# Performance work log

Measured on AMD Instinct MI355X. Metric: run time of the kernel, lower is better.

Reference implementation:

```python
import jax, jax.numpy as jnp
import numpy as np

N_NODES, N_FEAT, HIDDEN, N_EDGES, N_GRAPHS = 50000, 128, 64, 800000, 64
BN_EPS = 1e-5


def setup_inputs() -> dict:
    key = jax.random.key(0)
    ks = jax.random.split(key, 12)
    x = jax.random.normal(ks[0], (N_NODES, N_FEAT), jnp.float32)
    edge_index = jax.random.randint(ks[1], (2, N_EDGES), 0, N_NODES, jnp.int32)
    batch = jnp.sort(jax.random.randint(ks[2], (N_NODES,), 0, N_GRAPHS, jnp.int32))
    s_in = 1.0 / np.sqrt(N_FEAT)
    s_h = 1.0 / np.sqrt(HIDDEN)
    return {
        "x": x,
        "edge_index": edge_index,
        "batch": batch,
        "W_in": jax.random.normal(ks[3], (HIDDEN, N_FEAT), jnp.float32) * s_in,
        "W1": jax.random.normal(ks[4], (HIDDEN, N_FEAT), jnp.float32) * s_in,
        "b1": jnp.zeros((HIDDEN,), jnp.float32),
        "Ws": jax.random.normal(ks[5], (4, HIDDEN, HIDDEN), jnp.float32) * s_h,
        "bs": jnp.zeros((4, HIDDEN), jnp.float32),
        "bn_gamma": jnp.ones((5, HIDDEN), jnp.float32),
        "bn_beta": jnp.zeros((5, HIDDEN), jnp.float32),
        "bn_mean": jnp.zeros((5, HIDDEN), jnp.float32),
        "bn_var": jnp.ones((5, HIDDEN), jnp.float32),
        "lin_w": jax.random.normal(ks[6], (1, HIDDEN), jnp.float32) * s_h,
        "lin_b": jnp.zeros((1,), jnp.float32),
    }


def reference(x, edge_index, batch, W_in, W1, b1, Ws, bs, bn_gamma, bn_beta, bn_mean, bn_var, lin_w, lin_b):
    N = x.shape[0]
    # add self loops (GCNConv default), symmetric normalization D^-1/2 (A+I) D^-1/2
    loop = jnp.arange(N, dtype=edge_index.dtype)
    src = jnp.concatenate([edge_index[0], loop])  # [E+N]
    dst = jnp.concatenate([edge_index[1], loop])
    deg = jax.ops.segment_sum(jnp.ones_like(dst, jnp.float32), dst, num_segments=N)
    dinv = jax.lax.rsqrt(deg)  # deg >= 1 due to self-loops
    norm = dinv[src] * dinv[dst]  # [E+N]

    def gcn(h, W, b):
        h = h @ W.T                          # [N, H]
        msg = h[src] * norm[:, None]          # gather + edge scaling
        out = jax.ops.segment_sum(msg, dst, num_segments=N)  # scatter-add
        return out + b

    def bn(h, i):
        # eval-mode BatchNorm1d with running stats
        return (h - bn_mean[i]) * (bn_gamma[i] * jax.lax.rsqrt(bn_var[i] + BN_EPS)) + bn_beta[i]

    identity = x @ W_in.T  # input projection for residual
    # layer 1 (dropout = identity in eval)
    h = jax.nn.relu(bn(gcn(x, W1, b1), 0)) + identity
    # layers 2-4 with residual
    for i in range(3):
        h = jax.nn.relu(bn(gcn(h, Ws[i], bs[i]), i + 1)) + h
    # layer 5, no residual afterwards
    h = jax.nn.relu(bn(gcn(h, Ws[3], bs[3]), 4))

    # global mean pool over graphs
    sums = jax.ops.segment_sum(h, batch, num_segments=N_GRAPHS)
    cnts = jax.ops.segment_sum(jnp.ones((N,), jnp.float32), batch, num_segments=N_GRAPHS)
    pooled = sums / jnp.maximum(cnts, 1.0)[:, None]  # [G, H]
    return pooled @ lin_w.T + lin_b  # [G, 1]
```

## Files before the change

kernel.cpp:

```cpp
#include <hip/hip_runtime.h>
#include <hip/hip_fp16.h>

#define N_NODES 50000
#define N_FEAT  128
#define HID     64
#define N_EDGES 800000
#define N_GRAPHS 64
#define MAXDEG  64
#define BN_EPS  1e-5f
#define NB256(n) (((n) + 255) / 256)

__global__ __launch_bounds__(256) void k_zero(int* fill) {
    int i = blockIdx.x * 256 + threadIdx.x;
    if (i < N_NODES) fill[i] = 0;
}

#define GE_NB 2500
__global__ __launch_bounds__(256) void k_gemmedge(const int* __restrict__ ei,
                                                  int* fill, unsigned short* __restrict__ colp,
                                                  const float* __restrict__ x,
                                                  const float* __restrict__ W_in,
                                                  const float* __restrict__ W1,
                                                  float* __restrict__ h,
                                                  __half* __restrict__ g16) {
    __shared__ float4 Wt[2][8 * 65];
    __shared__ float4 xs[20 * 32];
    const int bid = blockIdx.x;
    const int t = threadIdx.x;

    const int ebase = bid * 320;
    int s1 = ei[ebase + t];
    int d1 = ei[N_EDGES + ebase + t];
    int k1 = atomicAdd(&fill[d1], 1);
    int s2 = 0, d2 = 0, k2 = MAXDEG;
    if (t < 64) {
        s2 = ei[ebase + 256 + t];
        d2 = ei[N_EDGES + ebase + 256 + t];
        k2 = atomicAdd(&fill[d2], 1);
    }

    const float4* W0v = (const float4*)W_in;
    const float4* W1v = (const float4*)W1;
    const int h2a = t >> 3, k4a = t & 7;
    const int h2b = h2a + 32;
    float4 w0a = W0v[h2a * 32 + k4a];
    float4 w1a = W1v[h2a * 32 + k4a];
    float4 w0b = W0v[h2b * 32 + k4a];
    float4 w1b = W1v[h2b * 32 + k4a];

    const int base = bid * 20;
    const float4* xv = (const float4*)(x + (long long)base * N_FEAT);
    for (int i = t; i < 20 * 32; i += 256) xs[i] = xv[i];

    const int hh = t & 63;
    const int ng = t >> 6;
    float4 a0[5], a1[5];
#pragma unroll
    for (int j = 0; j < 5; ++j) {
        a0[j] = make_float4(0.f, 0.f, 0.f, 0.f);
        a1[j] = make_float4(0.f, 0.f, 0.f, 0.f);
    }

    for (int c = 0; c < 32; c += 8) {
        __syncthreads();
        Wt[0][k4a * 65 + h2a] = w0a;  Wt[1][k4a * 65 + h2a] = w1a;
        Wt[0][k4a * 65 + h2b] = w0b;  Wt[1][k4a * 65 + h2b] = w1b;
        if (c + 8 < 32) {
            w0a = W0v[h2a * 32 + c + 8 + k4a]; w1a = W1v[h2a * 32 + c + 8 + k4a];
            w0b = W0v[h2b * 32 + c + 8 + k4a]; w1b = W1v[h2b * 32 + c + 8 + k4a];
        }
        __syncthreads();
#pragma unroll
        for (int k4 = 0; k4 < 8; ++k4) {
            float4 w0 = Wt[0][k4 * 65 + hh];
            float4 w1 = Wt[1][k4 * 65 + hh];
#pragma unroll
            for (int j = 0; j < 5; ++j) {
                float4 xx = xs[(ng + 4 * j) * 32 + c + k4];
                a0[j].x += w0.x * xx.x; a0[j].y += w0.y * xx.y;
                a0[j].z += w0.z * xx.z; a0[j].w += w0.w * xx.w;
                a1[j].x += w1.x * xx.x; a1[j].y += w1.y * xx.y;
                a1[j].z += w1.z * xx.z; a1[j].w += w1.w * xx.w;
            }
        }
    }
#pragma unroll
    for (int j = 0; j < 5; ++j) {
        int node = base + ng + 4 * j;
        h[node * HID + hh]   = a0[j].x + a0[j].y + a0[j].z + a0[j].w;
        g16[node * HID + hh] = __float2half(a1[j].x + a1[j].y + a1[j].z + a1[j].w);
    }

    if (k1 < MAXDEG) colp[d1 * MAXDEG + k1] = (unsigned short)s1;
    if (k2 < MAXDEG) colp[d2 * MAXDEG + k2] = (unsigned short)s2;
}

__device__ __forceinline__ void acc8s(const uint4 r, float* a, float s) {
    float2 f0 = __half22float2(*(const __half2*)&r.x);
    float2 f1 = __half22float2(*(const __half2*)&r.y);
    float2 f2 = __half22float2(*(const __half2*)&r.z);
    float2 f3 = __half22float2(*(const __half2*)&r.w);
    a[0] += s * f0.x; a[1] += s * f0.y; a[2] += s * f1.x; a[3] += s * f1.y;
    a[4] += s * f2.x; a[5] += s * f2.y; a[6] += s * f3.x; a[7] += s * f3.y;
}

template <bool NSCALE, bool DOGEMM>
__global__ __launch_bounds__(256) void k_gather_fused(const __half* __restrict__ gin,
                                                      const unsigned short* __restrict__ colp,
                                                      const int* __restrict__ fill,
                                                      const float* __restrict__ b,
                                                      const float* __restrict__ gamma,
                                                      const float* __restrict__ beta,
                                                      const float* __restrict__ mean,
                                                      const float* __restrict__ var,
                                                      const float4* __restrict__ res4,
                                                      float4* __restrict__ h4,
                                                      const float* __restrict__ W,
                                                      __half* __restrict__ gout) {
    __shared__ float4 Wt[DOGEMM ? 16 * 65 : 1];
    __shared__ float4 hrow[DOGEMM ? 32 * 17 : 1];

    const int t = threadIdx.x;
    const int wv = t >> 6;
    const int lane = t & 63;
    const int hh8 = lane & 7;
    const int sub = lane >> 3;
    const int nl = wv * 8 + sub;
    const int n = blockIdx.x * 32 + nl;
    const bool nvalid = (n < N_NODES);

    if (DOGEMM) {
        const float4* Wv = (const float4*)W;
        for (int i = t; i < HID * 16; i += 256) {
            int h2 = i >> 4, k4 = i & 15;
            Wt[k4 * 65 + h2] = Wv[i];
        }
        __syncthreads();
    }

    const uint4* gv = (const uint4*)gin;
    const int fl = nvalid ? fill[n] : 0;
    const int deg = fl < MAXDEG ? fl : MAXDEG;

    const uint4 vself = gv[(size_t)(nvalid ? n : 0) * 8 + hh8];
    float4 r0 = make_float4(0.f, 0.f, 0.f, 0.f), r1 = r0;
    if (res4 != nullptr && nvalid) {
        r0 = res4[(size_t)n * 16 + hh8 * 2];
        r1 = res4[(size_t)n * 16 + hh8 * 2 + 1];
    }

    float a[8];
#pragma unroll
    for (int i = 0; i < 8; ++i) a[i] = 0.f;

    const uint4* cp8 = (const uint4*)(colp + (size_t)n * MAXDEG);

#pragma unroll 1
    for (int rb = 0; rb < MAXDEG; rb += 8) {
        if (!__any(rb < deg)) break;
        if (rb < deg) {
            uint4 cc = cp8[rb >> 3];
            unsigned cw[4] = {cc.x, cc.y, cc.z, cc.w};
            int c[8]; float s[8]; uint4 v[8];
#pragma unroll
            for (int k = 0; k < 8; ++k) {
                bool pk = (rb + k) < deg;
                int col = (int)((cw[k >> 1] >> (16 * (k & 1))) & 0xFFFFu);
                c[k] = pk ? col : 0;
                if (NSCALE) s[k] = pk ? rsqrtf((float)fill[c[k]] + 1.0f) : 0.0f;
                else        s[k] = pk ? 1.0f : 0.0f;
            }
#pragma unroll
            for (int k = 0; k < 8; ++k) v[k] = gv[(size_t)c[k] * 8 + hh8];
#pragma unroll
            for (int k = 0; k < 8; ++k) acc8s(v[k], a, s[k]);
        }
    }

    const float di = rsqrtf((float)fl + 1.0f);
    if (nvalid) acc8s(vself, a, NSCALE ? di : 1.0f);

    float o[8];
    {
        float4 b0 = ((const float4*)b)[hh8 * 2],     b1 = ((const float4*)b)[hh8 * 2 + 1];
        float4 g0 = ((const float4*)gamma)[hh8 * 2], g1 = ((const float4*)gamma)[hh8 * 2 + 1];
        float4 e0 = ((const float4*)beta)[hh8 * 2],  e1 = ((const float4*)beta)[hh8 * 2 + 1];
        float4 m0 = ((const float4*)mean)[hh8 * 2],  m1 = ((const float4*)mean)[hh8 * 2 + 1];
        float4 v0 = ((const float4*)var)[hh8 * 2],   v1 = ((const float4*)var)[hh8 * 2 + 1];
        float bb[8] = {b0.x, b0.y, b0.z, b0.w, b1.x, b1.y, b1.z, b1.w};
        float gg[8] = {g0.x, g0.y, g0.z, g0.w, g1.x, g1.y, g1.z, g1.w};
        float ee[8] = {e0.x, e0.y, e0.z, e0.w, e1.x, e1.y, e1.z, e1.w};
        float mm[8] = {m0.x, m0.y, m0.z, m0.w, m1.x, m1.y, m1.z, m1.w};
        float vv[8] = {v0.x, v0.y, v0.z, v0.w, v1.x, v1.y, v1.z, v1.w};
#pragma unroll
        for (int i = 0; i < 8; ++i) {
            float sc = gg[i] * rsqrtf(vv[i] + BN_EPS);
            float sh = (bb[i] - mm[i]) * sc + ee[i];
            o[i] = fmaxf(fmaf(a[i] * di, sc, sh), 0.f);
        }
    }

    o[0] += r0.x; o[1] += r0.y; o[2] += r0.z; o[3] += r0.w;
    o[4] += r1.x; o[5] += r1.y; o[6] += r1.z; o[7] += r1.w;

    float4 lo = make_float4(o[0], o[1], o[2], o[3]);
    float4 hi = make_float4(o[4], o[5], o[6], o[7]);
    if (nvalid) {
        h4[(size_t)n * 16 + hh8 * 2]     = lo;
        h4[(size_t)n * 16 + hh8 * 2 + 1] = hi;
    }

    if (DOGEMM) {
        hrow[nl * 17 + hh8 * 2]     = lo;
        hrow[nl * 17 + hh8 * 2 + 1] = hi;
        const int hh = lane;
        const int nb = blockIdx.x * 32 + wv * 8;
        float acc[8];
#pragma unroll
        for (int s8 = 0; s8 < 8; ++s8) acc[s8] = 0.f;
#pragma unroll 2
        for (int k4 = 0; k4 < 16; ++k4) {
            float4 w = Wt[k4 * 65 + hh];
#pragma unroll
            for (int s8 = 0; s8 < 8; ++s8) {
                float4 hv = hrow[(wv * 8 + s8) * 17 + k4];
                acc[s8] += hv.x * w.x + hv.y * w.y + hv.z * w.z + hv.w * w.w;
            }
        }
#pragma unroll
        for (int s8 = 0; s8 < 8; ++s8) {
            int ns = nb + s8;
            if (ns < N_NODES) {
                float dd = rsqrtf((float)fill[ns] + 1.0f);
                gout[(size_t)ns * HID + hh] = __float2half(acc[s8] * dd);
            }
        }
    }
}

__device__ __forceinline__ int lowerb(const int* __restrict__ b, int val) {
    int lo = 0, hi = N_NODES;
    while (lo < hi) {
        int mid = (lo + hi) >> 1;
        if (b[mid] < val) lo = mid + 1; else hi = mid;
    }
    return lo;
}

__global__ __launch_bounds__(1024) void k_poolfinal(const float* __restrict__ h,
                                                    const int* __restrict__ batch,
                                                    const float* __restrict__ lin_w,
                                                    const float* __restrict__ lin_b,
                                                    float* __restrict__ out) {
    __shared__ float red[16][HID];
    int g = blockIdx.x;
    int w = threadIdx.x >> 6;
    int hh = threadIdx.x & 63;
    int start = lowerb(batch, g);
    int end = lowerb(batch, g + 1);
    int len = end - start;
    float acc = 0.f;
    for (int n = start + w; n < end; n += 16) acc += h[n * HID + hh];
    red[w][hh] = acc;
    __syncthreads();
    if (w == 0) {
        float s = 0.f;
#pragma unroll
        for (int i = 0; i < 16; ++i) s += red[i][hh];
        float c = fmaxf((float)len, 1.0f);
        float v = (s / c) * lin_w[hh];
#pragma unroll
        for (int off = 32; off > 0; off >>= 1) v += __shfl_down(v, off);
        if (hh == 0) out[g] = v + lin_b[0];
    }
}

extern "C" void kernel_launch(void* const* d_in, const int* in_sizes, int n_in,
                              void* d_out, int out_size, void* d_ws, size_t ws_size,
                              hipStream_t stream) {
    const float* x     = (const float*)d_in[0];
    const int*   ei    = (const int*)d_in[1];
    const int*   batch = (const int*)d_in[2];
    const float* W_in  = (const float*)d_in[3];
    const float* W1    = (const float*)d_in[4];
    const float* b1    = (const float*)d_in[5];
    const float* Ws    = (const float*)d_in[6];
    const float* bs_   = (const float*)d_in[7];
    const float* bn_g  = (const float*)d_in[8];
    const float* bn_b  = (const float*)d_in[9];
    const float* bn_m  = (const float*)d_in[10];
    const float* bn_v  = (const float*)d_in[11];
    const float* lin_w = (const float*)d_in[12];
    const float* lin_b = (const float*)d_in[13];
    float* out = (float*)d_out;

    char* q = (char*)d_ws;
    int*            fill = (int*)q;             q += (size_t)50048 * 4;
    unsigned short* colp = (unsigned short*)q;  q += (size_t)N_NODES * MAXDEG * 2;
    __half*         g16a = (__half*)q;          q += (size_t)N_NODES * HID * 2;
    __half*         g16b = (__half*)q;          q += (size_t)N_NODES * HID * 2;
    float*          h    = (float*)q;           q += (size_t)N_NODES * HID * 4;

    const int NB_N  = NB256(N_NODES);
    const int NB_GA = (N_NODES + 31) / 32;
    float4* h4 = (float4*)h;

    k_zero<<<NB_N, 256, 0, stream>>>(fill);
    k_gemmedge<<<GE_NB, 256, 0, stream>>>(ei, fill, colp, x, W_in, W1, h, g16a);

    k_gather_fused<true, true><<<NB_GA, 256, 0, stream>>>(
        g16a, colp, fill, b1, bn_g, bn_b, bn_m, bn_v,
        (const float4*)h, h4, Ws + 0 * HID * HID, g16b);

    k_gather_fused<false, true><<<NB_GA, 256, 0, stream>>>(
        g16b, colp, fill, bs_ + 0 * HID,
        bn_g + 1 * HID, bn_b + 1 * HID, bn_m + 1 * HID, bn_v + 1 * HID,
        (const float4*)h, h4, Ws + 1 * HID * HID, g16a);

    k_gather_fused<false, true><<<NB_GA, 256, 0, stream>>>(
        g16a, colp, fill, bs_ + 1 * HID,
        bn_g + 2 * HID, bn_b + 2 * HID, bn_m + 2 * HID, bn_v + 2 * HID,
        (const float4*)h, h4, Ws + 2 * HID * HID, g16b);

    k_gather_fused<false, true><<<NB_GA, 256, 0, stream>>>(
        g16b, colp, fill, bs_ + 2 * HID,
        bn_g + 3 * HID, bn_b + 3 * HID, bn_m + 3 * HID, bn_v + 3 * HID,
        (const float4*)h, h4, Ws + 3 * HID * HID, g16a);

    k_gather_fused<false, false><<<NB_GA, 256, 0, stream>>>(
        g16a, colp, fill, bs_ + 3 * HID,
        bn_g + 4 * HID, bn_b + 4 * HID, bn_m + 4 * HID, bn_v + 4 * HID,
        nullptr, h4, nullptr, nullptr);

    k_poolfinal<<<N_GRAPHS, 1024, 0, stream>>>(h, batch, lin_w, lin_b, out);
}
```

Before: 314.9 us.

## Software-pipeline neighbor gather with double-buffered 4-edge batches

```diff
diff --git a/kernel.cpp b/kernel.cpp
--- a/kernel.cpp
+++ b/kernel.cpp
@@ -102,6 +102,30 @@
     float2 f3 = __half22float2(*(const __half2*)&r.w);
     a[0] += s * f0.x; a[1] += s * f0.y; a[2] += s * f1.x; a[3] += s * f1.y;
     a[4] += s * f2.x; a[5] += s * f2.y; a[6] += s * f3.x; a[7] += s * f3.y;
+}
+
+template <bool NSCALE>
+__device__ __forceinline__ void unpack4(uint2 cc, int rb, int deg,
+                                        const int* __restrict__ fill,
+                                        int* c, float* s) {
+    unsigned cw[2] = {cc.x, cc.y};
+#pragma unroll
+    for (int k = 0; k < 4; ++k) {
+        bool pk = (rb + k) < deg;
+        int col = (int)((cw[k >> 1] >> (16 * (k & 1))) & 0xFFFFu);
+        c[k] = pk ? col : 0;
+        if (NSCALE) s[k] = pk ? rsqrtf((float)fill[c[k]] + 1.0f) : 0.0f;
+        else        s[k] = pk ? 1.0f : 0.0f;
+    }
+}
+__device__ __forceinline__ void issue4(const uint4* __restrict__ gv,
+                                       const int* c, int hh8, uint4* v) {
+#pragma unroll
+    for (int k = 0; k < 4; ++k) v[k] = gv[(size_t)c[k] * 8 + hh8];
+}
+__device__ __forceinline__ void accum4(const uint4* v, const float* s, float* a) {
+#pragma unroll
+    for (int k = 0; k < 4; ++k) acc8s(v[k], a, s[k]);
 }
 
 template <bool NSCALE, bool DOGEMM>
@@ -153,28 +177,31 @@
 #pragma unroll
     for (int i = 0; i < 8; ++i) a[i] = 0.f;
 
-    const uint4* cp8 = (const uint4*)(colp + (size_t)n * MAXDEG);
+    int nbw = (deg + 3) >> 2;
+#pragma unroll
+    for (int m = 8; m <= 32; m <<= 1) {
+        int o = __shfl_xor(nbw, m);
+        nbw = o > nbw ? o : nbw;
+    }
+
+    const uint2* cp4 = (const uint2*)(colp + (size_t)n * MAXDEG);
+
+    uint2 ccA = cp4[0];
+    uint2 ccB = cp4[1];
+    int cA[4], cB[4]; float sA[4], sB[4]; uint4 vA[4], vB[4];
+    unpack4<NSCALE>(ccA, 0, deg, fill, cA, sA);
+    issue4(gv, cA, hh8, vA);
 
 #pragma unroll 1
-    for (int rb = 0; rb < MAXDEG; rb += 8) {
-        if (!__any(rb < deg)) break;
-        if (rb < deg) {
-            uint4 cc = cp8[rb >> 3];
-            unsigned cw[4] = {cc.x, cc.y, cc.z, cc.w};
-            int c[8]; float s[8]; uint4 v[8];
-#pragma unroll
-            for (int k = 0; k < 8; ++k) {
-                bool pk = (rb + k) < deg;
-                int col = (int)((cw[k >> 1] >> (16 * (k & 1))) & 0xFFFFu);
-                c[k] = pk ? col : 0;
-                if (NSCALE) s[k] = pk ? rsqrtf((float)fill[c[k]] + 1.0f) : 0.0f;
-                else        s[k] = pk ? 1.0f : 0.0f;
-            }
-#pragma unroll
-            for (int k = 0; k < 8; ++k) v[k] = gv[(size_t)c[k] * 8 + hh8];
-#pragma unroll
-            for (int k = 0; k < 8; ++k) acc8s(v[k], a, s[k]);
-        }
+    for (int i = 0; i < nbw; i += 2) {
+        unpack4<NSCALE>(ccB, (i + 1) * 4, deg, fill, cB, sB);
+        issue4(gv, cB, hh8, vB);
+        ccA = cp4[(i + 2) & 15];
+        accum4(vA, sA, a);
+        unpack4<NSCALE>(ccA, (i + 2) * 4, deg, fill, cA, sA);
+        issue4(gv, cA, hh8, vA);
+        ccB = cp4[(i + 3) & 15];
+        accum4(vB, sB, a);
     }
 
     const float di = rsqrtf((float)fl + 1.0f);
```

Result: no change. 313.1 us (-0.6%).
